# Kernel optimization log

Measured on AMD Instinct MI355X. Metric: run time of the kernel, lower is better.

Reference implementation:

```python
import jax, jax.numpy as jnp
import numpy as np

B, S, D, H, KP, DK = 4, 2048, 1024, 16, 8, 3
DD = D // H
NEG = -1.0e9


def dense(x, W, b):
    return x @ W + b


def dw_conv_causal(x, w, b):
    # x: [B,S,D], w: [DK,D] per-channel kernel, b: [D]; left pad DK-1 zeros -> VALID conv
    xp = jnp.pad(x, ((0, 0), (DK - 1, 0), (0, 0)))
    y = b
    for t in range(DK):
        y = y + xp[:, t:t + S, :] * w[t]
    return y


def split_heads(x):
    return x.reshape(B, S, H, DD).transpose(0, 2, 1, 3)  # [B,H,S,DD]


def pool_causal(x):
    # left pad KP-1 zeros along seq, avg_pool window=stride=KP, VALID
    xp = jnp.pad(x, ((0, 0), (0, 0), (KP - 1, 0), (0, 0)))
    n = (S - 1) // KP + 1  # TF VALID output length
    return xp[:, :, :n * KP, :].reshape(B, H, n, KP, DD).mean(axis=3)


def forward(q, k, v, Wq, bq, Wk, bk, Wv, bv, Wup, bup, Wc, bc,
            wcq, bcq, wck, bck, wcv, bcv):
    norm = float(DD) ** -0.25
    qh = dense(q, Wq, bq) * norm
    kh = dense(k, Wk, bk) * norm
    vh = dense(v, Wv, bv)
    q_in = split_heads(dw_conv_causal(qh, wcq, bcq))
    k_in = split_heads(dw_conv_causal(kh, wck, bck))
    v_in = split_heads(dw_conv_causal(vh, wcv, bcv))
    qp = pool_causal(q_in)  # [B,H,n,DD]
    kp = pool_causal(k_in)
    vp = pool_causal(v_in)
    n = qp.shape[2]
    mask = NEG * (1.0 - jnp.tril(jnp.ones((n, n), dtype=qp.dtype)))
    logits = jnp.einsum('bhnd,bhmd->bhnm', qp, kp) + mask
    attn = jax.nn.softmax(logits, axis=-1)
    out = jnp.einsum('bhnm,bhmd->bhnd', attn, vp)  # [B,H,n,DD]
    up = jnp.repeat(out, KP, axis=2)[:, :, :S, :]  # upsample + crop
    up = dense(up, Wup, bup)
    merged = up.transpose(0, 2, 1, 3).reshape(B, S, D)
    return dense(merged, Wc, bc)


def setup_inputs() -> dict:
    key = jax.random.key(0)
    ks = jax.random.split(key, 20)
    w = lambda i, shp: jax.random.normal(ks[i], shp, dtype=jnp.float32) * 0.02
    return {
        'q': jax.random.normal(ks[0], (B, S, D), dtype=jnp.float32),
        'k': jax.random.normal(ks[1], (B, S, D), dtype=jnp.float32),
        'v': jax.random.normal(ks[2], (B, S, D), dtype=jnp.float32),
        'Wq': w(3, (D, D)), 'bq': jnp.zeros((D,), jnp.float32),
        'Wk': w(4, (D, D)), 'bk': jnp.zeros((D,), jnp.float32),
        'Wv': w(5, (D, D)), 'bv': jnp.zeros((D,), jnp.float32),
        'Wup': w(6, (DD, DD)), 'bup': jnp.zeros((DD,), jnp.float32),
        'Wc': w(7, (D, D)), 'bc': jnp.zeros((D,), jnp.float32),
        'wcq': w(8, (DK, D)), 'bcq': jnp.zeros((D,), jnp.float32),
        'wck': w(9, (DK, D)), 'bck': jnp.zeros((D,), jnp.float32),
        'wcv': w(10, (DK, D)), 'bcv': jnp.zeros((D,), jnp.float32),
    }


def reference(q, k, v, Wq, bq, Wk, bk, Wv, bv, Wup, bup, Wc, bc,
              wcq, bcq, wck, bck, wcv, bcv):
    return forward(q, k, v, Wq, bq, Wk, bk, Wv, bv, Wup, bup, Wc, bc,
                   wcq, bcq, wck, bck, wcv, bcv)
```

## Files before the change

kernel.cpp:

```cpp
#include <hip/hip_runtime.h>
#include <cstdint>

#define Bc  4
#define Sc  2048
#define Dc  1024
#define Hc  16
#define DDc 64
#define Nc  256

typedef unsigned short u16;
typedef unsigned int   u32;
typedef __bf16 bf16_t;
typedef bf16_t bf16x8 __attribute__((ext_vector_type(8)));
typedef float  f32x4  __attribute__((ext_vector_type(4)));

__device__ __forceinline__ u16 f2bf(float x) {
    u32 u = __float_as_uint(x);
    return (u16)((u + 0x7FFFu + ((u >> 16) & 1u)) >> 16);
}
__device__ __forceinline__ float bf2f(u16 x) {
    return __uint_as_float((u32)x << 16);
}

__device__ __forceinline__ void gload_lds16(const void* gp, void* lp) {
    __builtin_amdgcn_global_load_lds(
        reinterpret_cast<const __attribute__((address_space(1))) void*>(
            reinterpret_cast<uintptr_t>(gp)),
        reinterpret_cast<__attribute__((address_space(3))) void*>(
            reinterpret_cast<uintptr_t>(lp)),
        16, 0, 0);
}

__global__ __launch_bounds__(256) void cast_wt4_kernel(
    const float* __restrict__ Wq, const float* __restrict__ Wk,
    const float* __restrict__ Wv, const float* __restrict__ Wc,
    u16* __restrict__ Wt4)
{
    __shared__ float T[64][65];
    const int z = blockIdx.z;
    const float* W = (z == 0) ? Wq : (z == 1) ? Wk : (z == 2) ? Wv : Wc;
    u16* Wt = Wt4 + ((size_t)z << 20);
    const int k0 = blockIdx.y * 64, n0 = blockIdx.x * 64;
    const int c = threadIdx.x & 63, r4 = threadIdx.x >> 6;
    #pragma unroll
    for (int i = 0; i < 16; ++i) {
        int r = i * 4 + r4;
        T[r][c] = W[(size_t)(k0 + r) * 1024 + n0 + c];
    }
    __syncthreads();
    #pragma unroll
    for (int i = 0; i < 16; ++i) {
        int r = i * 4 + r4;
        Wt[(size_t)(n0 + r) * 1024 + k0 + c] = f2bf(T[c][r]);
    }
}

__global__ __launch_bounds__(256) void stage_kernel(
    const float* __restrict__ q, const float* __restrict__ k,
    const float* __restrict__ v, u16* __restrict__ R)
{
    int gid = blockIdx.x * 256 + threadIdx.x;
    int c = gid & 1023, t = (gid >> 10) & 255, b = (gid >> 18) & 3, inp = gid >> 20;
    const float* src = (inp == 0) ? q : (inp == 1) ? k : v;
    const float* Xb = src + (size_t)b * Sc * Dc + c;

    int sbase = (t << 3) - 9;
    float s8 = 0.f;
    #pragma unroll
    for (int i = 0; i < 8; ++i) {
        int s = sbase + i;
        s8 += (s >= 0) ? Xb[(size_t)s * Dc] : 0.f;
    }
    float xa = (t > 0) ? Xb[(size_t)((t << 3) - 1) * Dc] : 0.f;
    float xb = Xb[(size_t)(t << 3) * Dc];

    u32 lo = gid & 0xFFFFFu;
    size_t s0 = ((size_t)(inp * 3) << 20) + lo;
    R[s0]              = f2bf(s8);
    R[s0 + (1u << 20)] = f2bf(xa);
    R[s0 + (2u << 20)] = f2bf(xb);
}

__global__ __launch_bounds__(256) void gemm_sec(
    u16* __restrict__ Rall, const u16* __restrict__ Wt4)
{
    __shared__ __align__(16) u16 As[128 * 32];
    __shared__ __align__(16) u16 Bs[128 * 32];

    const int tid  = threadIdx.x;
    const int lane = tid & 63;
    const int wv   = tid >> 6;
    const int z    = blockIdx.z;
    const int inp  = z / 3;
    const int m0   = blockIdx.y * 128;
    const int n0   = blockIdx.x * 128;

    const char* Ab = (const char*)(Rall + ((size_t)z << 20));
    const char* Bb = (const char*)(Wt4 + ((size_t)inp << 20));

    const int wm   = (wv & 1) * 64;
    const int wn   = (wv >> 1) * 64;
    const int mi   = lane & 15;
    const int quad = lane >> 4;

    f32x4 acc[4][4];
    #pragma unroll
    for (int i = 0; i < 4; ++i)
        #pragma unroll
        for (int j = 0; j < 4; ++j)
            acc[i][j] = (f32x4){0.f, 0.f, 0.f, 0.f};

    const int ra0 = tid >> 2, cb = (tid & 3) * 16;
    char* AsB = (char*)As;
    char* BsB = (char*)Bs;

    for (int k0 = 0; k0 < 1024; k0 += 32) {
        const size_t kb = (size_t)k0 * 2;
        gload_lds16(Ab + ((size_t)(m0 + ra0)      << 11) + kb + cb, AsB + wv * 1024);
        gload_lds16(Ab + ((size_t)(m0 + 64 + ra0) << 11) + kb + cb, AsB + 4096 + wv * 1024);
        gload_lds16(Bb + ((size_t)(n0 + ra0)      << 11) + kb + cb, BsB + wv * 1024);
        gload_lds16(Bb + ((size_t)(n0 + 64 + ra0) << 11) + kb + cb, BsB + 4096 + wv * 1024);
        __syncthreads();

        bf16x8 af[4], bfr[4];
        #pragma unroll
        for (int i = 0; i < 4; ++i)
            af[i] = *reinterpret_cast<const bf16x8*>(&As[(wm + i * 16 + mi) * 32 + quad * 8]);
        #pragma unroll
        for (int j = 0; j < 4; ++j)
            bfr[j] = *reinterpret_cast<const bf16x8*>(&Bs[(wn + j * 16 + mi) * 32 + quad * 8]);

        #pragma unroll
        for (int i = 0; i < 4; ++i)
            #pragma unroll
            for (int j = 0; j < 4; ++j)
                acc[i][j] = __builtin_amdgcn_mfma_f32_16x16x32_bf16(af[i], bfr[j], acc[i][j], 0, 0, 0);

        __syncthreads();
    }

    u16* Cs = Rall + ((size_t)z << 20);
    #pragma unroll
    for (int j = 0; j < 4; ++j) {
        const int col = n0 + wn + j * 16 + mi;
        #pragma unroll
        for (int i = 0; i < 4; ++i) {
            const int row = m0 + wm + i * 16 + quad * 4;
            #pragma unroll
            for (int r = 0; r < 4; ++r)
                Cs[(size_t)(row + r) * 1024 + col] = f2bf(acc[i][j][r]);
        }
    }
}

__global__ __launch_bounds__(256) void combine_kernel(
    const u16* __restrict__ Y,
    const float* __restrict__ wcq, const float* __restrict__ wck, const float* __restrict__ wcv,
    const float* __restrict__ bcq, const float* __restrict__ bck, const float* __restrict__ bcv,
    const float* __restrict__ bq,  const float* __restrict__ bk,  const float* __restrict__ bv,
    float* __restrict__ pbase)
{
    int gid = blockIdx.x * 256 + threadIdx.x;
    int c = gid & 1023, t = (gid >> 10) & 255, b = (gid >> 18) & 3, inp = gid >> 20;
    const float* wc = (inp == 0) ? wcq : (inp == 1) ? wck : wcv;
    const float* bconv = (inp == 0) ? bcq : (inp == 1) ? bck : bcv;
    const float* bl = (inp == 0) ? bq : (inp == 1) ? bk : bv;
    const float nrm = (inp == 2) ? 1.0f : 0.35355339059327373f;

    float w0 = wc[c], w1 = wc[1024 + c], w2 = wc[2048 + c];
    float sumw = w0 + w1 + w2, w12 = w1 + w2;

    u32 lo = gid & 0xFFFFFu;
    size_t z0 = (size_t)(inp * 3) << 20;
    float Y0  = bf2f(Y[z0 + lo]);
    float Y1  = bf2f(Y[z0 + (1u << 20) + lo]);
    float Y2  = bf2f(Y[z0 + (2u << 20) + lo]);
    float Y1p = (t > 0) ? bf2f(Y[z0 + (1u << 20) + lo - 1024]) : 0.f;
    float Y2p = (t > 0) ? bf2f(Y[z0 + (2u << 20) + lo - 1024]) : 0.f;

    float data = sumw * Y0 + w12 * (Y1 - Y1p) + w2 * (Y2 - Y2p);

    float cnt = (t == 0) ? 1.f : 8.f;
    float n0  = (t == 0) ? 0.f : ((t == 1) ? 7.f : 8.f);
    float n1  = (t == 0) ? 0.f : 8.f;
    float n2  = (t == 0) ? 1.f : 8.f;
    float val = 0.125f * (cnt * bconv[c] + nrm * (bl[c] * (n0 * w0 + n1 * w1 + n2 * w2) + data));

    int h = c >> 6, d = c & 63;
    pbase[((size_t)inp << 20) + (((size_t)(b * 16 + h) * 256 + t) << 6) + d] = val;
}

__global__ __launch_bounds__(256, 2) void attn_kernel(
    const float* __restrict__ qp, const float* __restrict__ kp,
    const float* __restrict__ vp, float* __restrict__ ao)
{
    __shared__ float Ks[64 * 68];
    __shared__ float Vs[64 * 68];
    const int bh  = blockIdx.x >> 3;
    const int qt  = blockIdx.x & 7;
    const int tid = threadIdx.x;
    const int q   = tid >> 3;
    const int j   = tid & 7;
    const int qi  = qt * 32 + q;

    const float4* qrow = (const float4*)(qp + ((size_t)bh * Nc + qi) * DDc);
    float4 q4[16];
    #pragma unroll
    for (int i = 0; i < 16; ++i) q4[i] = qrow[i];

    float4 o4[16];
    #pragma unroll
    for (int i = 0; i < 16; ++i) o4[i] = make_float4(0.f, 0.f, 0.f, 0.f);
    float l = 0.f;

    const int ntiles = (qt >> 1) + 1;
    for (int tile = 0; tile < ntiles; ++tile) {
        const float4* ksrc = (const float4*)(kp + ((size_t)bh * Nc + tile * 64) * DDc);
        const float4* vsrc = (const float4*)(vp + ((size_t)bh * Nc + tile * 64) * DDc);
        __syncthreads();
        #pragma unroll
        for (int i = 0; i < 4; ++i) {
            int flat = tid + 256 * i;
            int row = flat >> 4, col = flat & 15;
            ((float4*)Ks)[row * 17 + col] = ksrc[flat];
            ((float4*)Vs)[row * 17 + col] = vsrc[flat];
        }
        __syncthreads();

        const int rel   = qi - tile * 64;
        const int mmEnd = (rel > 63) ? 63 : rel;
        for (int mm = j; mm <= mmEnd; mm += 8) {
            const float4* Krow = (const float4*)&Ks[mm * 68];
            float4 acc = make_float4(0.f, 0.f, 0.f, 0.f);
            #pragma unroll
            for (int i = 0; i < 16; ++i) {
                float4 k4 = Krow[i];
                acc.x += q4[i].x * k4.x;
                acc.y += q4[i].y * k4.y;
                acc.z += q4[i].z * k4.z;
                acc.w += q4[i].w * k4.w;
            }
            float s = (acc.x + acc.y) + (acc.z + acc.w);
            float e = __expf(s);
            l += e;
            const float4* Vrow = (const float4*)&Vs[mm * 68];
            #pragma unroll
            for (int i = 0; i < 16; ++i) {
                float4 v4 = Vrow[i];
                o4[i].x += e * v4.x;
                o4[i].y += e * v4.y;
                o4[i].z += e * v4.z;
                o4[i].w += e * v4.w;
            }
        }
    }

    float4 r8[8];
    #pragma unroll
    for (int i = 0; i < 8; ++i) {
        float4 send = (j & 4) ? o4[i] : o4[i + 8];
        float4 keep = (j & 4) ? o4[i + 8] : o4[i];
        float4 recv;
        recv.x = __shfl_xor(send.x, 4, 64);
        recv.y = __shfl_xor(send.y, 4, 64);
        recv.z = __shfl_xor(send.z, 4, 64);
        recv.w = __shfl_xor(send.w, 4, 64);
        r8[i] = make_float4(keep.x + recv.x, keep.y + recv.y, keep.z + recv.z, keep.w + recv.w);
    }
    float4 r4[4];
    #pragma unroll
    for (int i = 0; i < 4; ++i) {
        float4 send = (j & 2) ? r8[i] : r8[i + 4];
        float4 keep = (j & 2) ? r8[i + 4] : r8[i];
        float4 recv;
        recv.x = __shfl_xor(send.x, 2, 64);
        recv.y = __shfl_xor(send.y, 2, 64);
        recv.z = __shfl_xor(send.z, 2, 64);
        recv.w = __shfl_xor(send.w, 2, 64);
        r4[i] = make_float4(keep.x + recv.x, keep.y + recv.y, keep.z + recv.z, keep.w + recv.w);
    }
    float4 r2[2];
    #pragma unroll
    for (int i = 0; i < 2; ++i) {
        float4 send = (j & 1) ? r4[i] : r4[i + 2];
        float4 keep = (j & 1) ? r4[i + 2] : r4[i];
        float4 recv;
        recv.x = __shfl_xor(send.x, 1, 64);
        recv.y = __shfl_xor(send.y, 1, 64);
        recv.z = __shfl_xor(send.z, 1, 64);
        recv.w = __shfl_xor(send.w, 1, 64);
        r2[i] = make_float4(keep.x + recv.x, keep.y + recv.y, keep.z + recv.z, keep.w + recv.w);
    }

    l += __shfl_xor(l, 1, 64);
    l += __shfl_xor(l, 2, 64);
    l += __shfl_xor(l, 4, 64);
    float inv = 1.0f / l;

    float4* orow = (float4*)(ao + ((size_t)bh * Nc + qi) * DDc);
    orow[2 * j]     = make_float4(r2[0].x * inv, r2[0].y * inv, r2[0].z * inv, r2[0].w * inv);
    orow[2 * j + 1] = make_float4(r2[1].x * inv, r2[1].y * inv, r2[1].z * inv, r2[1].w * inv);
}

__global__ __launch_bounds__(256) void updense_kernel(
    const float* __restrict__ ao, const float* __restrict__ Wup,
    const float* __restrict__ bup, u16* __restrict__ ms)
{
    __shared__ float Ws[64 * 64];
    __shared__ float rows[4 * 64];
    const int tid = threadIdx.x;

    #pragma unroll
    for (int i = 0; i < 4; ++i)
        ((float4*)Ws)[tid + 256 * i] = ((const float4*)Wup)[tid + 256 * i];
    rows[tid] = ao[(size_t)blockIdx.x * 256 + tid];
    __syncthreads();

    const int r = tid >> 6, dp = tid & 63;
    const int R = blockIdx.x * 4 + r;
    const int b = R >> 12;
    const int h = (R >> 8) & 15;
    const int m = R & 255;

    float acc = bup[dp];
    #pragma unroll
    for (int d = 0; d < 64; ++d)
        acc += rows[r * 64 + d] * Ws[d * 64 + dp];

    ms[((size_t)(b * Nc + m) << 10) + h * 64 + dp] = f2bf(acc);
}

__global__ __launch_bounds__(256) void gemm_final(
    const u16* __restrict__ A, const u16* __restrict__ Bt,
    const float* __restrict__ bias, float* __restrict__ out)
{
    __shared__ __align__(16) u16 As[128 * 32];
    __shared__ __align__(16) u16 Bs[128 * 32];

    const int tid  = threadIdx.x;
    const int lane = tid & 63;
    const int wv   = tid >> 6;
    const int m0   = blockIdx.y * 128;
    const int n0   = blockIdx.x * 128;

    const int wm   = (wv & 1) * 64;
    const int wn   = (wv >> 1) * 64;
    const int mi   = lane & 15;
    const int quad = lane >> 4;

    f32x4 acc[4][4];
    #pragma unroll
    for (int i = 0; i < 4; ++i)
        #pragma unroll
        for (int j = 0; j < 4; ++j)
            acc[i][j] = (f32x4){0.f, 0.f, 0.f, 0.f};

    const char* Ab = (const char*)A;
    const char* Bb = (const char*)Bt;
    const int ra0 = tid >> 2, cb = (tid & 3) * 16;
    char* AsB = (char*)As;
    char* BsB = (char*)Bs;

    for (int k0 = 0; k0 < 1024; k0 += 32) {
        const size_t kb = (size_t)k0 * 2;
        gload_lds16(Ab + ((size_t)(m0 + ra0)      << 11) + kb + cb, AsB + wv * 1024);
        gload_lds16(Ab + ((size_t)(m0 + 64 + ra0) << 11) + kb + cb, AsB + 4096 + wv * 1024);
        gload_lds16(Bb + ((size_t)(n0 + ra0)      << 11) + kb + cb, BsB + wv * 1024);
        gload_lds16(Bb + ((size_t)(n0 + 64 + ra0) << 11) + kb + cb, BsB + 4096 + wv * 1024);
        __syncthreads();

        bf16x8 af[4], bfr[4];
        #pragma unroll
        for (int i = 0; i < 4; ++i)
            af[i] = *reinterpret_cast<const bf16x8*>(&As[(wm + i * 16 + mi) * 32 + quad * 8]);
        #pragma unroll
        for (int j = 0; j < 4; ++j)
            bfr[j] = *reinterpret_cast<const bf16x8*>(&Bs[(wn + j * 16 + mi) * 32 + quad * 8]);

        #pragma unroll
        for (int i = 0; i < 4; ++i)
            #pragma unroll
            for (int j = 0; j < 4; ++j)
                acc[i][j] = __builtin_amdgcn_mfma_f32_16x16x32_bf16(af[i], bfr[j], acc[i][j], 0, 0, 0);

        __syncthreads();
    }

    #pragma unroll
    for (int j = 0; j < 4; ++j) {
        const int col = n0 + wn + j * 16 + mi;
        const float bv = bias[col];
        #pragma unroll
        for (int i = 0; i < 4; ++i) {
            const int row = m0 + wm + i * 16 + quad * 4;
            #pragma unroll
            for (int r = 0; r < 4; ++r) {
                const int rr = row + r;
                const int b = rr >> 8, t = rr & 255;
                float val = acc[i][j][r] + bv;
                float* po = out + (((size_t)b * Sc + (t << 3)) << 10) + col;
                #pragma unroll
                for (int rep = 0; rep < 8; ++rep)
                    po[(size_t)rep << 10] = val;
            }
        }
    }
}

extern "C" void kernel_launch(void* const* d_in, const int* in_sizes, int n_in,
                              void* d_out, int out_size, void* d_ws, size_t ws_size,
                              hipStream_t stream) {
    const float* q   = (const float*)d_in[0];
    const float* k   = (const float*)d_in[1];
    const float* v   = (const float*)d_in[2];
    const float* Wq  = (const float*)d_in[3];
    const float* bq  = (const float*)d_in[4];
    const float* Wk  = (const float*)d_in[5];
    const float* bk  = (const float*)d_in[6];
    const float* Wv  = (const float*)d_in[7];
    const float* bv  = (const float*)d_in[8];
    const float* Wup = (const float*)d_in[9];
    const float* bup = (const float*)d_in[10];
    const float* Wc  = (const float*)d_in[11];
    const float* bc  = (const float*)d_in[12];
    const float* wcq = (const float*)d_in[13];
    const float* bcq = (const float*)d_in[14];
    const float* wck = (const float*)d_in[15];
    const float* bck = (const float*)d_in[16];
    const float* wcv = (const float*)d_in[17];
    const float* bcv = (const float*)d_in[18];

    u16* Rall = (u16*)d_out;

    char* wsb = (char*)d_ws;
    u16*   Wt4  = (u16*)wsb;
    float* qp   = (float*)(wsb + 8388608);
    float* kp   = qp + (1 << 20);
    float* vp   = kp + (1 << 20);
    float* ao   = (float*)(wsb + 20971520);
    u16*   ms   = (u16*)(wsb + 25165824);

    cast_wt4_kernel<<<dim3(16, 16, 4), 256, 0, stream>>>(Wq, Wk, Wv, Wc, Wt4);
    stage_kernel<<<12288, 256, 0, stream>>>(q, k, v, Rall);
    gemm_sec<<<dim3(8, 8, 9), 256, 0, stream>>>(Rall, Wt4);
    combine_kernel<<<12288, 256, 0, stream>>>(Rall, wcq, wck, wcv, bcq, bck, bcv,
                                              bq, bk, bv, qp);
    attn_kernel<<<Bc * Hc * 8, 256, 0, stream>>>(qp, kp, vp, ao);
    updense_kernel<<<(Bc * Hc * Nc) / 4, 256, 0, stream>>>(ao, Wup, bup, ms);
    gemm_final<<<dim3(8, 8), 256, 0, stream>>>(ms, Wt4 + ((size_t)3 << 20), bc, (float*)d_out);
}
```

Measured before the change: 296.3 us.

## Move pooled attention to bf16 MFMA and vectorize staging loads

Replaces the scalar fp32 causal attention kernel with a bf16 MFMA kernel. Q and K are stored in bf16 and V is stored transposed, padded with a ones row so the softmax denominator falls out of the PV matmul. The combine kernel now writes these bf16 layouts, and a new small kernel fills the padding rows. The staging kernel is vectorized to float4 loads and packed bf16 stores. The change adds bf16 rounding of the attention inputs and probabilities. Only 64 blocks are launched for attention, which leaves many compute units idle.

Result: faster. 284.9 us (-3.8%).

```diff
diff --git a/kernel.cpp b/kernel.cpp
--- a/kernel.cpp
+++ b/kernel.cpp
@@ -17,6 +17,9 @@
 __device__ __forceinline__ u16 f2bf(float x) {
     u32 u = __float_as_uint(x);
     return (u16)((u + 0x7FFFu + ((u >> 16) & 1u)) >> 16);
+}
+__device__ __forceinline__ u32 pack2(float a, float b) {
+    return (u32)f2bf(a) | ((u32)f2bf(b) << 16);
 }
 __device__ __forceinline__ float bf2f(u16 x) {
     return __uint_as_float((u32)x << 16);
@@ -60,25 +63,28 @@
     const float* __restrict__ v, u16* __restrict__ R)
 {
     int gid = blockIdx.x * 256 + threadIdx.x;
-    int c = gid & 1023, t = (gid >> 10) & 255, b = (gid >> 18) & 3, inp = gid >> 20;
+    int c4 = gid & 255, t = (gid >> 8) & 255, b = (gid >> 16) & 3, inp = gid >> 18;
     const float* src = (inp == 0) ? q : (inp == 1) ? k : v;
-    const float* Xb = src + (size_t)b * Sc * Dc + c;
+    const float4* Xb = (const float4*)(src + (size_t)b * Sc * Dc) + c4;
 
     int sbase = (t << 3) - 9;
-    float s8 = 0.f;
+    float4 s8 = make_float4(0.f, 0.f, 0.f, 0.f);
     #pragma unroll
     for (int i = 0; i < 8; ++i) {
         int s = sbase + i;
-        s8 += (s >= 0) ? Xb[(size_t)s * Dc] : 0.f;
-    }
-    float xa = (t > 0) ? Xb[(size_t)((t << 3) - 1) * Dc] : 0.f;
-    float xb = Xb[(size_t)(t << 3) * Dc];
-
-    u32 lo = gid & 0xFFFFFu;
-    size_t s0 = ((size_t)(inp * 3) << 20) + lo;
-    R[s0]              = f2bf(s8);
-    R[s0 + (1u << 20)] = f2bf(xa);
-    R[s0 + (2u << 20)] = f2bf(xb);
+        if (s >= 0) {
+            float4 x = Xb[(size_t)s << 8];
+            s8.x += x.x; s8.y += x.y; s8.z += x.z; s8.w += x.w;
+        }
+    }
+    float4 xa = (t > 0) ? Xb[(size_t)((t << 3) - 1) << 8]
+                        : make_float4(0.f, 0.f, 0.f, 0.f);
+    float4 xb = Xb[(size_t)(t << 3) << 8];
+
+    size_t s0 = ((size_t)(inp * 3) << 20) + (((u32)(b * 256 + t)) << 10) + c4 * 4;
+    *(uint2*)(R + s0)               = make_uint2(pack2(s8.x, s8.y), pack2(s8.z, s8.w));
+    *(uint2*)(R + s0 + (1u << 20))  = make_uint2(pack2(xa.x, xa.y), pack2(xa.z, xa.w));
+    *(uint2*)(R + s0 + (2u << 20))  = make_uint2(pack2(xb.x, xb.y), pack2(xb.z, xb.w));
 }
 
 __global__ __launch_bounds__(256) void gemm_sec(
@@ -158,7 +164,7 @@
     const float* __restrict__ wcq, const float* __restrict__ wck, const float* __restrict__ wcv,
     const float* __restrict__ bcq, const float* __restrict__ bck, const float* __restrict__ bcv,
     const float* __restrict__ bq,  const float* __restrict__ bk,  const float* __restrict__ bv,
-    float* __restrict__ pbase)
+    u16* __restrict__ qb, u16* __restrict__ kb, u16* __restrict__ vt)
 {
     int gid = blockIdx.x * 256 + threadIdx.x;
     int c = gid & 1023, t = (gid >> 10) & 255, b = (gid >> 18) & 3, inp = gid >> 20;
@@ -187,119 +193,135 @@
     float val = 0.125f * (cnt * bconv[c] + nrm * (bl[c] * (n0 * w0 + n1 * w1 + n2 * w2) + data));
 
     int h = c >> 6, d = c & 63;
-    pbase[((size_t)inp << 20) + (((size_t)(b * 16 + h) * 256 + t) << 6) + d] = val;
-}
-
-__global__ __launch_bounds__(256, 2) void attn_kernel(
-    const float* __restrict__ qp, const float* __restrict__ kp,
-    const float* __restrict__ vp, float* __restrict__ ao)
-{
-    __shared__ float Ks[64 * 68];
-    __shared__ float Vs[64 * 68];
-    const int bh  = blockIdx.x >> 3;
-    const int qt  = blockIdx.x & 7;
+    int bh = b * 16 + h;
+    u16 bfv = f2bf(val);
+    if (inp == 0)
+        qb[(((size_t)bh * 256 + t) << 6) + d] = bfv;
+    else if (inp == 1)
+        kb[(((size_t)bh * 256 + t) << 6) + d] = bfv;
+    else
+        vt[(size_t)bh * 80 * 256 + (size_t)d * 256 + t] = bfv;
+}
+
+__global__ __launch_bounds__(256) void vpad_kernel(u16* __restrict__ vt)
+{
+    const int bh = blockIdx.x;
     const int tid = threadIdx.x;
-    const int q   = tid >> 3;
-    const int j   = tid & 7;
-    const int qi  = qt * 32 + q;
-
-    const float4* qrow = (const float4*)(qp + ((size_t)bh * Nc + qi) * DDc);
-    float4 q4[16];
-    #pragma unroll
-    for (int i = 0; i < 16; ++i) q4[i] = qrow[i];
-
-    float4 o4[16];
-    #pragma unroll
-    for (int i = 0; i < 16; ++i) o4[i] = make_float4(0.f, 0.f, 0.f, 0.f);
-    float l = 0.f;
-
-    const int ntiles = (qt >> 1) + 1;
-    for (int tile = 0; tile < ntiles; ++tile) {
-        const float4* ksrc = (const float4*)(kp + ((size_t)bh * Nc + tile * 64) * DDc);
-        const float4* vsrc = (const float4*)(vp + ((size_t)bh * Nc + tile * 64) * DDc);
-        __syncthreads();
-        #pragma unroll
-        for (int i = 0; i < 4; ++i) {
-            int flat = tid + 256 * i;
-            int row = flat >> 4, col = flat & 15;
-            ((float4*)Ks)[row * 17 + col] = ksrc[flat];
-            ((float4*)Vs)[row * 17 + col] = vsrc[flat];
+    const int rr = tid >> 4;
+    const int c0 = (tid & 15) * 16;
+    u32 fill = (rr == 0) ? 0x3F803F80u : 0u;
+    uint4 val = make_uint4(fill, fill, fill, fill);
+    uint4* p = (uint4*)(vt + (size_t)bh * 80 * 256 + (size_t)(64 + rr) * 256 + c0);
+    p[0] = val;
+    p[1] = val;
+}
+
+__global__ __launch_bounds__(256) void attn_mfma(
+    const u16* __restrict__ qb, const u16* __restrict__ kb,
+    const u16* __restrict__ vt, float* __restrict__ ao)
+{
+    __shared__ __align__(16) u16 Ps[4][64 * 72];
+    const int bh   = blockIdx.x;
+    const int tid  = threadIdx.x;
+    const int wv   = tid >> 6;
+    const int lane = tid & 63;
+    const int mi   = lane & 15;
+    const int quad = lane >> 4;
+
+    const u16* Qb = qb + (((size_t)bh * 256 + wv * 64) << 6);
+    const u16* Kb = kb + ((size_t)bh << 14);
+    const u16* Vt = vt + (size_t)bh * 80 * 256;
+    u16* P = Ps[wv];
+
+    bf16x8 qf[4][2];
+    #pragma unroll
+    for (int it = 0; it < 4; ++it)
+        #pragma unroll
+        for (int kc = 0; kc < 2; ++kc)
+            qf[it][kc] = *(const bf16x8*)(Qb + ((it * 16 + mi) << 6) + kc * 32 + quad * 8);
+
+    f32x4 o[4][5];
+    #pragma unroll
+    for (int it = 0; it < 4; ++it)
+        #pragma unroll
+        for (int jn = 0; jn < 5; ++jn)
+            o[it][jn] = (f32x4){0.f, 0.f, 0.f, 0.f};
+
+    for (int kt = 0; kt <= wv; ++kt) {
+        bf16x8 kf[4][2];
+        #pragma unroll
+        for (int jt = 0; jt < 4; ++jt)
+            #pragma unroll
+            for (int kc = 0; kc < 2; ++kc)
+                kf[jt][kc] = *(const bf16x8*)(Kb + ((kt * 64 + jt * 16 + mi) << 6) + kc * 32 + quad * 8);
+
+        f32x4 s[4][4];
+        #pragma unroll
+        for (int it = 0; it < 4; ++it)
+            #pragma unroll
+            for (int jt = 0; jt < 4; ++jt)
+                s[it][jt] = (f32x4){0.f, 0.f, 0.f, 0.f};
+        #pragma unroll
+        for (int kc = 0; kc < 2; ++kc)
+            #pragma unroll
+            for (int it = 0; it < 4; ++it)
+                #pragma unroll
+                for (int jt = 0; jt < 4; ++jt)
+                    s[it][jt] = __builtin_amdgcn_mfma_f32_16x16x32_bf16(qf[it][kc], kf[jt][kc], s[it][jt], 0, 0, 0);
+
+        const bool diag = (kt == wv);
+        #pragma unroll
+        for (int it = 0; it < 4; ++it)
+            #pragma unroll
+            for (int jt = 0; jt < 4; ++jt)
+                #pragma unroll
+                for (int r = 0; r < 4; ++r) {
+                    int qrow = it * 16 + quad * 4 + r;
+                    int kcol = jt * 16 + mi;
+                    float e = __expf(s[it][jt][r]);
+                    if (diag && kcol > qrow) e = 0.f;
+                    P[qrow * 72 + kcol] = f2bf(e);
+                }
+
+        bf16x8 pf[4][2];
+        #pragma unroll
+        for (int it = 0; it < 4; ++it)
+            #pragma unroll
+            for (int kc = 0; kc < 2; ++kc)
+                pf[it][kc] = *(const bf16x8*)(P + (it * 16 + mi) * 72 + kc * 32 + quad * 8);
+
+        bf16x8 vf[5][2];
+        #pragma unroll
+        for (int jn = 0; jn < 5; ++jn)
+            #pragma unroll
+            for (int kc = 0; kc < 2; ++kc)
+                vf[jn][kc] = *(const bf16x8*)(Vt + (size_t)(jn * 16 + mi) * 256 + kt * 64 + kc * 32 + quad * 8);
+
+        #pragma unroll
+        for (int kc = 0; kc < 2; ++kc)
+            #pragma unroll
+            for (int it = 0; it < 4; ++it)
+                #pragma unroll
+                for (int jn = 0; jn < 5; ++jn)
+                    o[it][jn] = __builtin_amdgcn_mfma_f32_16x16x32_bf16(pf[it][kc], vf[jn][kc], o[it][jn], 0, 0, 0);
+    }
+
+    #pragma unroll
+    for (int it = 0; it < 4; ++it) {
+        float inv[4];
+        #pragma unroll
+        for (int r = 0; r < 4; ++r) {
+            float lv = __shfl(o[it][4][r], (lane & 48));
+            inv[r] = 1.0f / lv;
         }
-        __syncthreads();
-
-        const int rel   = qi - tile * 64;
-        const int mmEnd = (rel > 63) ? 63 : rel;
-        for (int mm = j; mm <= mmEnd; mm += 8) {
-            const float4* Krow = (const float4*)&Ks[mm * 68];
-            float4 acc = make_float4(0.f, 0.f, 0.f, 0.f);
-            #pragma unroll
-            for (int i = 0; i < 16; ++i) {
-                float4 k4 = Krow[i];
-                acc.x += q4[i].x * k4.x;
-                acc.y += q4[i].y * k4.y;
-                acc.z += q4[i].z * k4.z;
-                acc.w += q4[i].w * k4.w;
+        #pragma unroll
+        for (int jn = 0; jn < 4; ++jn)
+            #pragma unroll
+            for (int r = 0; r < 4; ++r) {
+                int row = wv * 64 + it * 16 + quad * 4 + r;
+                ao[(((size_t)bh * 256 + row) << 6) + jn * 16 + mi] = o[it][jn][r] * inv[r];
             }
-            float s = (acc.x + acc.y) + (acc.z + acc.w);
-            float e = __expf(s);
-            l += e;
-            const float4* Vrow = (const float4*)&Vs[mm * 68];
-            #pragma unroll
-            for (int i = 0; i < 16; ++i) {
-                float4 v4 = Vrow[i];
-                o4[i].x += e * v4.x;
-                o4[i].y += e * v4.y;
-                o4[i].z += e * v4.z;
-                o4[i].w += e * v4.w;
-            }
-        }
-    }
-
-    float4 r8[8];
-    #pragma unroll
-    for (int i = 0; i < 8; ++i) {
-        float4 send = (j & 4) ? o4[i] : o4[i + 8];
-        float4 keep = (j & 4) ? o4[i + 8] : o4[i];
-        float4 recv;
-        recv.x = __shfl_xor(send.x, 4, 64);
-        recv.y = __shfl_xor(send.y, 4, 64);
-        recv.z = __shfl_xor(send.z, 4, 64);
-        recv.w = __shfl_xor(send.w, 4, 64);
-        r8[i] = make_float4(keep.x + recv.x, keep.y + recv.y, keep.z + recv.z, keep.w + recv.w);
-    }
-    float4 r4[4];
-    #pragma unroll
-    for (int i = 0; i < 4; ++i) {
-        float4 send = (j & 2) ? r8[i] : r8[i + 4];
-        float4 keep = (j & 2) ? r8[i + 4] : r8[i];
-        float4 recv;
-        recv.x = __shfl_xor(send.x, 2, 64);
-        recv.y = __shfl_xor(send.y, 2, 64);
-        recv.z = __shfl_xor(send.z, 2, 64);
-        recv.w = __shfl_xor(send.w, 2, 64);
-        r4[i] = make_float4(keep.x + recv.x, keep.y + recv.y, keep.z + recv.z, keep.w + recv.w);
-    }
-    float4 r2[2];
-    #pragma unroll
-    for (int i = 0; i < 2; ++i) {
-        float4 send = (j & 1) ? r4[i] : r4[i + 2];
-        float4 keep = (j & 1) ? r4[i + 2] : r4[i];
-        float4 recv;
-        recv.x = __shfl_xor(send.x, 1, 64);
-        recv.y = __shfl_xor(send.y, 1, 64);
-        recv.z = __shfl_xor(send.z, 1, 64);
-        recv.w = __shfl_xor(send.w, 1, 64);
-        r2[i] = make_float4(keep.x + recv.x, keep.y + recv.y, keep.z + recv.z, keep.w + recv.w);
-    }
-
-    l += __shfl_xor(l, 1, 64);
-    l += __shfl_xor(l, 2, 64);
-    l += __shfl_xor(l, 4, 64);
-    float inv = 1.0f / l;
-
-    float4* orow = (float4*)(ao + ((size_t)bh * Nc + qi) * DDc);
-    orow[2 * j]     = make_float4(r2[0].x * inv, r2[0].y * inv, r2[0].z * inv, r2[0].w * inv);
-    orow[2 * j + 1] = make_float4(r2[1].x * inv, r2[1].y * inv, r2[1].z * inv, r2[1].w * inv);
+    }
 }
 
 __global__ __launch_bounds__(256) void updense_kernel(
@@ -433,19 +455,20 @@
     u16* Rall = (u16*)d_out;
 
     char* wsb = (char*)d_ws;
-    u16*   Wt4  = (u16*)wsb;
-    float* qp   = (float*)(wsb + 8388608);
-    float* kp   = qp + (1 << 20);
-    float* vp   = kp + (1 << 20);
-    float* ao   = (float*)(wsb + 20971520);
-    u16*   ms   = (u16*)(wsb + 25165824);
+    u16*   Wt4 = (u16*)wsb;
+    u16*   qb  = (u16*)(wsb + 8388608);
+    u16*   kb  = (u16*)(wsb + 10485760);
+    u16*   vt  = (u16*)(wsb + 12582912);
+    float* ao  = (float*)(wsb + 15204352);
+    u16*   ms  = (u16*)(wsb + 19398656);
 
     cast_wt4_kernel<<<dim3(16, 16, 4), 256, 0, stream>>>(Wq, Wk, Wv, Wc, Wt4);
-    stage_kernel<<<12288, 256, 0, stream>>>(q, k, v, Rall);
+    stage_kernel<<<3072, 256, 0, stream>>>(q, k, v, Rall);
     gemm_sec<<<dim3(8, 8, 9), 256, 0, stream>>>(Rall, Wt4);
     combine_kernel<<<12288, 256, 0, stream>>>(Rall, wcq, wck, wcv, bcq, bck, bcv,
-                                              bq, bk, bv, qp);
-    attn_kernel<<<Bc * Hc * 8, 256, 0, stream>>>(qp, kp, vp, ao);
+                                              bq, bk, bv, qb, kb, vt);
+    vpad_kernel<<<64, 256, 0, stream>>>(vt);
+    attn_mfma<<<64, 256, 0, stream>>>(qb, kb, vt, ao);
     updense_kernel<<<(Bc * Hc * Nc) / 4, 256, 0, stream>>>(ao, Wup, bup, ms);
     gemm_final<<<dim3(8, 8), 256, 0, stream>>>(ms, Wt4 + ((size_t)3 << 20), bc, (float*)d_out);
 }
```
